# Performance work log

Hardware: AMD Instinct MI355X
Metric: run time of the kernel (lower is better)

The kernel has to match this reference:

```python
import jax, jax.numpy as jnp
import numpy as np

N = 100000      # nodes
E = 1600000     # edges (avg degree 16)
F_IN = 128      # node feature dim
F_OUT = 128     # GCN output dim


def setup_inputs() -> dict:
    key = jax.random.key(0)
    ks = jax.random.split(key, 11)
    s = 0.05  # weight scale to keep activations sane
    return {
        "x": jax.random.normal(ks[0], (N, F_IN), jnp.float32),
        "edge_index": jax.random.randint(ks[1], (2, E), 0, N, jnp.int32),
        "W": jax.random.normal(ks[2], (F_IN, F_OUT), jnp.float32) * s,
        "p": jax.random.normal(ks[3], (F_IN,), jnp.float32),
        "w_ih": jax.random.normal(ks[4], (3 * F_OUT, F_IN), jnp.float32) * s,
        "w_hh": jax.random.normal(ks[5], (3 * F_OUT, F_OUT), jnp.float32) * s,
        "b_ih": jax.random.normal(ks[6], (3 * F_OUT,), jnp.float32) * s,
        "b_hh": jax.random.normal(ks[7], (3 * F_OUT,), jnp.float32) * s,
        "conv_bias": jax.random.normal(ks[8], (F_OUT,), jnp.float32) * s,
        "lin_w": jax.random.normal(ks[9], (1, F_OUT), jnp.float32) * s,
        "lin_b": jax.random.normal(ks[10], (1,), jnp.float32) * s,
    }


def reference(x, edge_index, W, p, w_ih, w_hh, b_ih, b_hh, conv_bias, lin_w, lin_b):
    n_nodes = x.shape[0]
    k, H = W.shape  # k = F_IN rows, H = F_OUT hidden size

    # --- TopK summarize: pick k nodes, gate by tanh(score) -> X_tilde [k, F_IN]
    scores = x @ p / jnp.linalg.norm(p)
    top_vals, top_idx = jax.lax.top_k(scores, k)
    x_tilde = x[top_idx] * jnp.tanh(top_vals)[:, None]

    # --- one GRU step evolving W (hidden state = rows of W)
    gi = x_tilde @ w_ih.T + b_ih   # [k, 3H]
    gh = W @ w_hh.T + b_hh         # [k, 3H]
    r = jax.nn.sigmoid(gi[:, :H] + gh[:, :H])
    z = jax.nn.sigmoid(gi[:, H:2 * H] + gh[:, H:2 * H])
    n = jnp.tanh(gi[:, 2 * H:] + r * gh[:, 2 * H:])
    W_new = (1.0 - z) * n + z * W  # [F_IN, F_OUT]

    # --- GCN conv with fixed W: sym-normalized adjacency with self loops
    row, col = edge_index[0], edge_index[1]
    deg = jax.ops.segment_sum(jnp.ones_like(row, dtype=x.dtype), col,
                              num_segments=n_nodes) + 1.0  # +1 for self loop
    dinv = jax.lax.rsqrt(deg)
    xw = x @ W_new                                   # [N, F_OUT]
    coef = dinv[row] * dinv[col]                     # [E]
    agg = jax.ops.segment_sum(xw[row] * coef[:, None], col, num_segments=n_nodes)
    agg = agg + xw * (dinv * dinv)[:, None] + conv_bias  # self-loop term + bias

    # --- head: ReLU + Linear(F_OUT, 1)
    h = jax.nn.relu(agg)
    return h @ lin_w.T + lin_b  # [N, 1]
```

## Files before the change

### kernel.cpp

```cpp
#include <hip/hip_runtime.h>
#include <math.h>

#define N_NODES 100000
#define N_EDGES 1600000
#define F 128

#define BSH 8
#define NBUCK 391
#define BCAP 5120
#define PB_EDGES 2048
#define NB_PART 782
#define NB_SCORES 6250
#define NB_COLLECT 392

typedef unsigned int u32;
typedef unsigned short u16;
typedef __attribute__((ext_vector_type(8))) short short8;
typedef __attribute__((ext_vector_type(4))) float floatx4;
typedef __attribute__((ext_vector_type(2))) float f32x2;


__device__ __forceinline__ u32 key_of(float s) {
    u32 u = __float_as_uint(s);
    return (u & 0x80000000u) ? ~u : (u | 0x80000000u);
}

__device__ __forceinline__ float wave_reduce(float v) {
    #pragma unroll
    for (int off = 32; off > 0; off >>= 1) v += __shfl_down(v, off, 64);
    return v;
}

__device__ __forceinline__ u16 f2bf(float f) {
    u32 u = __float_as_uint(f);
    u += 0x7fffu + ((u >> 16) & 1u);
    return (u16)(u >> 16);
}

__device__ __forceinline__ float bflo(u32 b) { return __uint_as_float(b << 16); }
__device__ __forceinline__ float bfhi(u32 b) { return __uint_as_float(b & 0xffff0000u); }

__device__ __forceinline__ void pk_acc(f32x2& acc, u32 u) {
    f32x2 v; v.x = bflo(u); v.y = bfhi(u);
    asm("v_pk_add_f32 %0, %1, %0" : "+v"(acc) : "v"(v));
}
__device__ __forceinline__ void pk_add2(f32x2& a, f32x2 b) {
    asm("v_pk_add_f32 %0, %1, %0" : "+v"(a) : "v"(b));
}


__global__ __launch_bounds__(256) void k_part(const int* __restrict__ ei,
                                              u32* __restrict__ gcur,
                                              u32* __restrict__ pairs) {
    __shared__ u32 lh[NBUCK];
    __shared__ u32 lbase[NBUCK];
    int t = threadIdx.x;
    int e0 = blockIdx.x * PB_EDGES;
    int e1 = e0 + PB_EDGES; if (e1 > N_EDGES) e1 = N_EDGES;
    for (int i = t; i < NBUCK; i += 256) lh[i] = 0u;
    __syncthreads();
    for (int e = e0 + t; e < e1; e += 256)
        atomicAdd(&lh[((u32)ei[N_EDGES + e]) >> BSH], 1u);
    __syncthreads();
    for (int b = t; b < NBUCK; b += 256) {
        u32 c = lh[b];
        lbase[b] = c ? atomicAdd(&gcur[b], c) : 0u;
        lh[b] = 0u;
    }
    __syncthreads();
    for (int e = e0 + t; e < e1; e += 256) {
        u32 d = (u32)ei[N_EDGES + e];
        u32 b = d >> BSH;
        u32 pos = lbase[b] + atomicAdd(&lh[b], 1u);
        pairs[(size_t)b * BCAP + pos] = ((d & 255u) << 17) | (u32)ei[e];
    }
}


__global__ __launch_bounds__(256) void k_scores(const float* __restrict__ x,
                                                const float* __restrict__ p,
                                                float* __restrict__ scores,
                                                u32* __restrict__ hist16) {
    int wave = threadIdx.x >> 6;
    int lane = threadIdx.x & 63;
    int q = lane >> 4, sub = lane & 15;
    int node = blockIdx.x * 16 + wave * 4 + q;
    const float* xr = &x[(size_t)node * F + sub * 8];
    float4 v0 = *(const float4*)xr;
    float4 v1 = *(const float4*)(xr + 4);
    float4 p0 = *(const float4*)&p[sub * 8];
    float4 p1 = *(const float4*)&p[sub * 8 + 4];
    float d = v0.x * p0.x + v0.y * p0.y + v0.z * p0.z + v0.w * p0.w
            + v1.x * p1.x + v1.y * p1.y + v1.z * p1.z + v1.w * p1.w;
    #pragma unroll
    for (int off = 1; off < 16; off <<= 1) d += __shfl_xor(d, off, 64);
    if (sub == 0) {
        scores[node] = d;
        atomicAdd(&hist16[key_of(d) >> 16], 1u);
    }
}


__global__ __launch_bounds__(1024) void k_scan16(const u32* __restrict__ hist16,
                                                 u32* __restrict__ state) {
    __shared__ u32 a[1024];
    int t = threadIdx.x;
    const uint4* h4 = (const uint4*)hist16;
    u32 local = 0;
    #pragma unroll
    for (int i = 0; i < 16; i++) {
        uint4 v = h4[t * 16 + i];
        local += v.x + v.y + v.z + v.w;
    }
    a[t] = local;
    __syncthreads();
    for (int off = 1; off < 1024; off <<= 1) {
        u32 add = (t + off < 1024) ? a[t + off] : 0u;
        __syncthreads();
        a[t] += add;
        __syncthreads();
    }
    u32 S_above = (t == 1023) ? 0u : a[t + 1];
    if (S_above < 128u && a[t] >= 128u) {
        u32 cum = S_above;
        for (int v = t * 64 + 63; v >= t * 64; v--) {
            cum += hist16[v];
            if (cum >= 128u) { state[0] = (u32)v; break; }
        }
    }
}


__global__ __launch_bounds__(256) void k_mid(const float* __restrict__ scores,
                                             u32* __restrict__ state,
                                             u32* __restrict__ cand,
                                             const u32* __restrict__ pairs,
                                             const u32* __restrict__ gcur,
                                             u32* __restrict__ offs,
                                             float* __restrict__ dinv,
                                             u32* __restrict__ ebuf) {
    if (blockIdx.x < NB_COLLECT) {
        u32 T = state[0] << 16;
        int i = blockIdx.x * 256 + threadIdx.x;
        if (i < N_NODES) {
            if (key_of(scores[i]) >= T) {
                u32 pos = atomicAdd(&state[2], 1u);
                if (pos < 2048u) cand[pos] = (u32)i;
            }
        }
    } else {
        __shared__ u32 h[256];
        __shared__ u32 sc[256];
        __shared__ u32 ps[512];
        int b = blockIdx.x - NB_COLLECT, t = threadIdx.x;
        ps[t]       = (t < NBUCK)       ? gcur[t]       : 0u;
        ps[t + 256] = (t + 256 < NBUCK) ? gcur[t + 256] : 0u;
        __syncthreads();
        for (int off = 1; off < 512; off <<= 1) {
            int i0 = t, i1 = t + 256;
            u32 v0 = (i0 >= off) ? ps[i0 - off] : 0u;
            u32 v1 = (i1 >= off) ? ps[i1 - off] : 0u;
            __syncthreads();
            ps[i0] += v0; ps[i1] += v1;
            __syncthreads();
        }
        u32 base = ps[b] - gcur[b];
        u32 cnt  = gcur[b];
        const u32* seg = pairs + (size_t)b * BCAP;
        u32 lo = (u32)b << BSH;
        h[t] = 0u;
        __syncthreads();
        for (u32 i = t; i < cnt; i += 256)
            atomicAdd(&h[seg[i] >> 17], 1u);
        __syncthreads();
        sc[t] = h[t];
        __syncthreads();
        for (int off = 1; off < 256; off <<= 1) {
            u32 v = (t >= off) ? sc[t - off] : 0u;
            __syncthreads();
            sc[t] += v;
            __syncthreads();
        }
        int nn = N_NODES - (int)lo;
        if (t < nn) {
            u32 c = h[t];
            offs[lo + t] = base + (sc[t] - c);
            dinv[lo + t] = rsqrtf((float)c + 1.0f);
        }
        u32 excl = sc[t] - h[t];
        __syncthreads();
        sc[t] = excl;
        __syncthreads();
        for (u32 i = t; i < cnt; i += 256) {
            u32 pr = seg[i];
            u32 pos = base + atomicAdd(&sc[pr >> 17], 1u);
            ebuf[pos] = pr & 0x1ffffu;
        }
        if (b == 0 && t == 0) offs[N_NODES] = N_EDGES;
    }
}

__global__ void k_assemble16(const float* __restrict__ scores, const float* __restrict__ p,
                             const u32* __restrict__ state, const u32* __restrict__ cand,
                             u32* __restrict__ top_idx, float* __restrict__ gate) {
    __shared__ u32 ci[2048];
    __shared__ float csc[2048];
    __shared__ float s_inv;
    int t = threadIdx.x;
    if (t < 64) {
        float2 pv = *(const float2*)&p[t * 2];
        float d = pv.x * pv.x + pv.y * pv.y;
        d = wave_reduce(d);
        if (t == 0) s_inv = rsqrtf(d);
    }
    u32 nc = state[2]; if (nc > 2048u) nc = 2048u;
    for (u32 i = t; i < nc; i += 256) { u32 ix = cand[i]; ci[i] = ix; csc[i] = scores[ix]; }
    __syncthreads();
    for (u32 i = t; i < nc; i += 256) {
        u32 myk = key_of(csc[i]);
        u32 myi = ci[i];
        int rank = 0;
        for (u32 j = 0; j < nc; j++) {
            u32 ok = key_of(csc[j]);
            rank += (int)((ok > myk) || (ok == myk && ci[j] < myi));
        }
        if (rank < 128) {
            top_idx[rank] = myi;
            gate[rank] = tanhf(csc[i] * s_inv);
        }
    }
}


__global__ __launch_bounds__(256) void k_ggemm(const float* __restrict__ x,
                                               const float* __restrict__ W,
                                               const float* __restrict__ w_ih,
                                               const float* __restrict__ w_hh,
                                               const u32* __restrict__ top_idx,
                                               const float* __restrict__ gate,
                                               float* __restrict__ G) {
    __shared__ float As[32][128];
    __shared__ float Bs[64][131];
    int t = threadIdx.x;
    int k0 = blockIdx.x * 32;
    int by = blockIdx.y;
    int j0 = by * 64;
    bool is_gi = (by < 6);
    #pragma unroll
    for (int i = 0; i < 4; i++) {
        int l = t + i * 256;
        int row = l >> 5, c4 = l & 31;
        float4 v;
        if (is_gi) {
            u32 idx = top_idx[k0 + row];
            float gt = gate[k0 + row];
            v = *(const float4*)&x[(size_t)idx * F + c4 * 4];
            v.x *= gt; v.y *= gt; v.z *= gt; v.w *= gt;
        } else {
            v = *(const float4*)&W[(k0 + row) * F + c4 * 4];
        }
        *(float4*)&As[row][c4 * 4] = v;
    }
    const float* mat = is_gi ? w_ih : w_hh;
    int jbase = is_gi ? j0 : (j0 - 384);
    #pragma unroll
    for (int i = 0; i < 8; i++) {
        int l = t + i * 256;
        int row = l >> 5, c4 = l & 31;
        float4 v = *(const float4*)&mat[(jbase + row) * F + c4 * 4];
        Bs[row][c4 * 4 + 0] = v.x; Bs[row][c4 * 4 + 1] = v.y;
        Bs[row][c4 * 4 + 2] = v.z; Bs[row][c4 * 4 + 3] = v.w;
    }
    __syncthreads();
    int ty = t >> 5, tx = t & 31;
    float acc[4][2] = {};
    #pragma unroll 4
    for (int f = 0; f < 128; f++) {
        float b0 = Bs[tx * 2][f], b1 = Bs[tx * 2 + 1][f];
        #pragma unroll
        for (int i = 0; i < 4; i++) {
            float a = As[ty * 4 + i][f];
            acc[i][0] += a * b0;
            acc[i][1] += a * b1;
        }
    }
    #pragma unroll
    for (int i = 0; i < 4; i++) {
        int k = k0 + ty * 4 + i;
        G[(size_t)k * 768 + j0 + tx * 2 + 0] = acc[i][0];
        G[(size_t)k * 768 + j0 + tx * 2 + 1] = acc[i][1];
    }
}


__global__ void k_gate(const float* __restrict__ G, const float* __restrict__ W,
                       const float* __restrict__ b_ih, const float* __restrict__ b_hh,
                       float* __restrict__ Wnew, u16* __restrict__ Bfrag) {
    int idx = blockIdx.x * blockDim.x + threadIdx.x;
    int k = idx >> 7, h = idx & 127;
    const float* gk = &G[(size_t)k * 768];
    float gir = gk[h]       + b_ih[h];
    float giz = gk[128 + h] + b_ih[128 + h];
    float gin = gk[256 + h] + b_ih[256 + h];
    float ghr = gk[384 + h] + b_hh[h];
    float ghz = gk[512 + h] + b_hh[128 + h];
    float ghn = gk[640 + h] + b_hh[256 + h];
    float wv  = W[k * F + h];
    float rg = 1.0f / (1.0f + expf(-(gir + ghr)));
    float z  = 1.0f / (1.0f + expf(-(giz + ghz)));
    float n  = tanhf(gin + rg * ghn);
    float val = (1.0f - z) * n + z * wv;
    Wnew[k * F + h] = val;
    int nb = h >> 4, kc = k >> 5, q = (k >> 3) & 3, m = h & 15, jj = k & 7;
    Bfrag[(((nb * 4 + kc) * 64) + q * 16 + m) * 8 + jj] = f2bf(val);
}


__global__ __launch_bounds__(256) void k_gemm(const float* __restrict__ x,
                                              const u16* __restrict__ Bfrag,
                                              const float* __restrict__ dinv,
                                              u16* __restrict__ yw) {
    __shared__ __align__(16) u16 As[8448];
    int t = threadIdx.x;
    int r0 = blockIdx.x * 64;
    #pragma unroll
    for (int i = 0; i < 8; i++) {
        int l = t + i * 256;
        int row = l >> 5, c4 = l & 31;
        int f0 = c4 * 4;
        float4 v = {0.f, 0.f, 0.f, 0.f};
        if (r0 + row < N_NODES) v = *(const float4*)&x[(size_t)(r0 + row) * F + f0];
        int widx = (((row >> 4) * 4 + (f0 >> 5)) * 64 + ((f0 >> 3) & 3) * 16 + (row & 15)) * 8
                   + (f0 & 7);
        ushort4 s4;
        s4.x = f2bf(v.x); s4.y = f2bf(v.y); s4.z = f2bf(v.z); s4.w = f2bf(v.w);
        *(ushort4*)&As[widx] = s4;
    }
    __syncthreads();

    int wv = t >> 6, lane = t & 63;
    int q = lane >> 4, m = lane & 15;
    floatx4 acc[8] = {};
    #pragma unroll
    for (int kc = 0; kc < 4; kc++) {
        short8 a = *(const short8*)&As[((wv * 4 + kc) * 64 + lane) * 8];
        #pragma unroll
        for (int nb = 0; nb < 8; nb++) {
            short8 bfr = *(const short8*)&Bfrag[((nb * 4 + kc) * 64 + lane) * 8];
            acc[nb] = __builtin_amdgcn_mfma_f32_16x16x32_bf16(a, bfr, acc[nb], 0, 0, 0);
        }
    }
    __syncthreads();

    float d[4];
    #pragma unroll
    for (int reg = 0; reg < 4; reg++) {
        int gr = r0 + wv * 16 + q * 4 + reg;
        d[reg] = (gr < N_NODES) ? dinv[gr] : 0.f;
    }
    #pragma unroll
    for (int nb = 0; nb < 8; nb++) {
        #pragma unroll
        for (int reg = 0; reg < 4; reg++) {
            int row = wv * 16 + q * 4 + reg;
            As[row * 132 + nb * 16 + m] = f2bf(acc[nb][reg] * d[reg]);
        }
    }
    __syncthreads();
    {
        int row = t >> 2, segi = t & 3;
        int gr = r0 + row;
        if (gr < N_NODES) {
            const uint2* src = (const uint2*)&As[row * 132 + segi * 32];
            uint2* dst = (uint2*)&yw[(size_t)gr * F + segi * 32];
            #pragma unroll
            for (int i = 0; i < 8; i++) dst[i] = src[i];
        }
    }
}


#define EDGE_GROUP(J) {                                                      \
    u32 r = ebuf[(J) + q];                                                   \
    uint4 bb = *(const uint4*)&yw32[(size_t)r * 64 + sub * 4];               \
    pk_acc(a01, bb.x); pk_acc(a23, bb.y);                                    \
    pk_acc(a45, bb.z); pk_acc(a67, bb.w); }

#define BFLY(A) {                                                            \
    f32x2 tb;                                                                \
    tb.x = __shfl_xor(A.x, 16, 64); tb.y = __shfl_xor(A.y, 16, 64);          \
    pk_add2(A, tb);                                                          \
    tb.x = __shfl_xor(A.x, 32, 64); tb.y = __shfl_xor(A.y, 32, 64);          \
    pk_add2(A, tb); }

__global__ void k_gather(const u32* __restrict__ yw32, const u32* __restrict__ offs,
                         const u32* __restrict__ ebuf, const float* __restrict__ dinv,
                         const float* __restrict__ conv_bias, const float* __restrict__ lin_w,
                         const float* __restrict__ lin_b, float* __restrict__ out) {
    int c = blockIdx.x * 4 + (threadIdx.x >> 6);
    if (c >= N_NODES) return;
    int lane = threadIdx.x & 63;
    int q = lane >> 4, sub = lane & 15;
    u32 jbeg = offs[c], jend = offs[c + 1];
    f32x2 a01 = {0.f, 0.f}, a23 = {0.f, 0.f}, a45 = {0.f, 0.f}, a67 = {0.f, 0.f};
    u32 j = jbeg;
    for (; j + 16 <= jend; j += 16) {
        EDGE_GROUP(j) EDGE_GROUP(j + 4) EDGE_GROUP(j + 8) EDGE_GROUP(j + 12)
    }
    for (; j + 4 <= jend; j += 4) EDGE_GROUP(j)
    u32 rem = jend - j;
    if (rem) {
        u32 idx = ((u32)q < rem) ? (j + q) : j;
        u32 r = ebuf[idx];
        uint4 bb = *(const uint4*)&yw32[(size_t)r * 64 + sub * 4];
        if ((u32)q < rem) {
            pk_acc(a01, bb.x); pk_acc(a23, bb.y);
            pk_acc(a45, bb.z); pk_acc(a67, bb.w);
        }
    }
    BFLY(a01) BFLY(a23) BFLY(a45) BFLY(a67)
    float dc = dinv[c];
    uint4 sb = *(const uint4*)&yw32[(size_t)c * 64 + sub * 4];
    float4 cb0 = *(const float4*)&conv_bias[sub * 8];
    float4 cb1 = *(const float4*)&conv_bias[sub * 8 + 4];
    float4 lw0 = *(const float4*)&lin_w[sub * 8];
    float4 lw1 = *(const float4*)&lin_w[sub * 8 + 4];
    float h0 = fmaxf(dc * (a01.x + bflo(sb.x)) + cb0.x, 0.f);
    float h1 = fmaxf(dc * (a01.y + bfhi(sb.x)) + cb0.y, 0.f);
    float h2 = fmaxf(dc * (a23.x + bflo(sb.y)) + cb0.z, 0.f);
    float h3 = fmaxf(dc * (a23.y + bfhi(sb.y)) + cb0.w, 0.f);
    float h4 = fmaxf(dc * (a45.x + bflo(sb.z)) + cb1.x, 0.f);
    float h5 = fmaxf(dc * (a45.y + bfhi(sb.z)) + cb1.y, 0.f);
    float h6 = fmaxf(dc * (a67.x + bflo(sb.w)) + cb1.z, 0.f);
    float h7 = fmaxf(dc * (a67.y + bfhi(sb.w)) + cb1.w, 0.f);
    float part = (h0 * lw0.x + h1 * lw0.y + h2 * lw0.z + h3 * lw0.w)
               + (h4 * lw1.x + h5 * lw1.y + h6 * lw1.z + h7 * lw1.w);
    #pragma unroll
    for (int off = 8; off > 0; off >>= 1) part += __shfl_down(part, off, 64);
    if (lane == 0) out[c] = part + lin_b[0];
}


extern "C" void kernel_launch(void* const* d_in, const int* in_sizes, int n_in,
                              void* d_out, int out_size, void* d_ws, size_t ws_size,
                              hipStream_t stream) {
    const float* x         = (const float*)d_in[0];
    const int*   ei        = (const int*)  d_in[1];
    const float* W         = (const float*)d_in[2];
    const float* p         = (const float*)d_in[3];
    const float* w_ih      = (const float*)d_in[4];
    const float* w_hh      = (const float*)d_in[5];
    const float* b_ih      = (const float*)d_in[6];
    const float* b_hh      = (const float*)d_in[7];
    const float* conv_bias = (const float*)d_in[8];
    const float* lin_w     = (const float*)d_in[9];
    const float* lin_b     = (const float*)d_in[10];
    float* out = (float*)d_out;

    u32*   w  = (u32*)d_ws;
    float* wf = (float*)d_ws;

    const size_t SCORES_W = 0;
    const size_t DINV_W   = 100096;
    const size_t OFFS_W   = 200192;
    const size_t HIST16_W = 300288;
    const size_t STATE_W  = 365824;
    const size_t GCUR_W   = 365832;
    const size_t CAND_W   = 366224;
    const size_t TOPI_W   = 368272;
    const size_t GATE_W   = 368400;
    const size_t WNEW_W   = 368528;
    const size_t BFRAG_W  = 384912;
    const size_t PAIRS_W  = 389008;
    const size_t EBUF_W   = 2400000;
    const size_t YW_W     = 4000000;

    float* scores  = wf + SCORES_W;
    float* dinv    = wf + DINV_W;
    u32*   offs    = w  + OFFS_W;
    u32*   hist16  = w  + HIST16_W;
    u32*   state   = w  + STATE_W;
    u32*   gcur    = w  + GCUR_W;
    u32*   cand    = w  + CAND_W;
    u32*   top_idx = w  + TOPI_W;
    float* gate    = wf + GATE_W;
    float* Wnew    = wf + WNEW_W;
    u16*   Bfrag   = (u16*)(w + BFRAG_W);
    u32*   pairs   = w  + PAIRS_W;
    float* G       = wf + PAIRS_W;
    u32*   ebuf    = w  + EBUF_W;
    u16*   yw      = (u16*)(w + YW_W);
    u32*   yw32    = w + YW_W;

    hipMemsetAsync(hist16, 0, (65536 + 8 + NBUCK) * sizeof(u32), stream);

    k_part<<<NB_PART, 256, 0, stream>>>(ei, gcur, pairs);
    k_scores<<<NB_SCORES, 256, 0, stream>>>(x, p, scores, hist16);
    k_scan16<<<1, 1024, 0, stream>>>(hist16, state);
    k_mid<<<NB_COLLECT + NBUCK, 256, 0, stream>>>(scores, state, cand, pairs, gcur,
                                                  offs, dinv, ebuf);
    k_assemble16<<<1, 256, 0, stream>>>(scores, p, state, cand, top_idx, gate);

    k_ggemm<<<dim3(4, 12), 256, 0, stream>>>(x, W, w_ih, w_hh, top_idx, gate, G);
    k_gate<<<64, 256, 0, stream>>>(G, W, b_ih, b_hh, Wnew, Bfrag);

    k_gemm<<<1563, 256, 0, stream>>>(x, Bfrag, dinv, yw);

    k_gather<<<25000, 256, 0, stream>>>(yw32, offs, ebuf, dinv, conv_bias, lin_w,
                                        lin_b, out);
}
```

Before: 328.0 us.

## Fuse edge partition with score pass and move top-k selection into one block

Merges the edge-bucketing and score kernels into one launch, and drops the global 16-bit histogram and its atomics. Top-k threshold selection now runs in a single 1024-thread block using two-level 12-bit radix histograms in shared memory, then collects candidates. A second block of the same launch computes the bucket prefix that k_mid previously recomputed in every block. This cuts kernel launches, the large memset and global atomics, but it puts a serial single-block pass over all 100k scores on the critical path.

```diff
diff --git a/kernel.cpp b/kernel.cpp
--- a/kernel.cpp
+++ b/kernel.cpp
@@ -10,8 +10,7 @@
 #define BCAP 5120
 #define PB_EDGES 2048
 #define NB_PART 782
-#define NB_SCORES 6250
-#define NB_COLLECT 392
+#define NB_SCORES 1563
 
 typedef unsigned int u32;
 typedef unsigned short u16;
@@ -49,174 +48,158 @@
 }
 
 
-__global__ __launch_bounds__(256) void k_part(const int* __restrict__ ei,
-                                              u32* __restrict__ gcur,
-                                              u32* __restrict__ pairs) {
-    __shared__ u32 lh[NBUCK];
-    __shared__ u32 lbase[NBUCK];
+__global__ void k_front(const float* __restrict__ x, const float* __restrict__ p,
+                        const int* __restrict__ ei, float* __restrict__ scores,
+                        u32* __restrict__ gcur, u32* __restrict__ pairs) {
+    if (blockIdx.x < NB_PART) {
+        __shared__ u32 lh[NBUCK];
+        __shared__ u32 lbase[NBUCK];
+        int t = threadIdx.x;
+        int e0 = blockIdx.x * PB_EDGES;
+        int e1 = e0 + PB_EDGES; if (e1 > N_EDGES) e1 = N_EDGES;
+        for (int i = t; i < NBUCK; i += 256) lh[i] = 0u;
+        __syncthreads();
+        for (int e = e0 + t; e < e1; e += 256)
+            atomicAdd(&lh[((u32)ei[N_EDGES + e]) >> BSH], 1u);
+        __syncthreads();
+        for (int b = t; b < NBUCK; b += 256) {
+            u32 c = lh[b];
+            lbase[b] = c ? atomicAdd(&gcur[b], c) : 0u;
+            lh[b] = 0u;
+        }
+        __syncthreads();
+        for (int e = e0 + t; e < e1; e += 256) {
+            u32 d = (u32)ei[N_EDGES + e];
+            u32 b = d >> BSH;
+            u32 pos = lbase[b] + atomicAdd(&lh[b], 1u);
+            pairs[(size_t)b * BCAP + pos] = ((d & 255u) << 17) | (u32)ei[e];
+        }
+    } else {
+        int sb = blockIdx.x - NB_PART;
+        int wave = threadIdx.x >> 6;
+        int lane = threadIdx.x & 63;
+        int q = lane >> 4, sub = lane & 15;
+        int nb0 = sb * 64 + wave * 16 + q;
+        float4 p0 = *(const float4*)&p[sub * 8];
+        float4 p1 = *(const float4*)&p[sub * 8 + 4];
+        #pragma unroll
+        for (int r = 0; r < 4; r++) {
+            int node = nb0 + r * 4;
+            if (node >= N_NODES) continue;
+            const float* xr = &x[(size_t)node * F + sub * 8];
+            float4 v0 = *(const float4*)xr;
+            float4 v1 = *(const float4*)(xr + 4);
+            float d = v0.x * p0.x + v0.y * p0.y + v0.z * p0.z + v0.w * p0.w
+                    + v1.x * p1.x + v1.y * p1.y + v1.z * p1.z + v1.w * p1.w;
+            #pragma unroll
+            for (int off = 1; off < 16; off <<= 1) d += __shfl_xor(d, off, 64);
+            if (sub == 0) scores[node] = d;
+        }
+    }
+}
+
+
+__global__ __launch_bounds__(1024) void k_select(const float* __restrict__ scores,
+                                                 const float* __restrict__ p,
+                                                 u32* __restrict__ top_idx,
+                                                 float* __restrict__ gate,
+                                                 const u32* __restrict__ gcur,
+                                                 u32* __restrict__ bbase) {
     int t = threadIdx.x;
-    int e0 = blockIdx.x * PB_EDGES;
-    int e1 = e0 + PB_EDGES; if (e1 > N_EDGES) e1 = N_EDGES;
-    for (int i = t; i < NBUCK; i += 256) lh[i] = 0u;
-    __syncthreads();
-    for (int e = e0 + t; e < e1; e += 256)
-        atomicAdd(&lh[((u32)ei[N_EDGES + e]) >> BSH], 1u);
-    __syncthreads();
-    for (int b = t; b < NBUCK; b += 256) {
-        u32 c = lh[b];
-        lbase[b] = c ? atomicAdd(&gcur[b], c) : 0u;
-        lh[b] = 0u;
-    }
-    __syncthreads();
-    for (int e = e0 + t; e < e1; e += 256) {
-        u32 d = (u32)ei[N_EDGES + e];
-        u32 b = d >> BSH;
-        u32 pos = lbase[b] + atomicAdd(&lh[b], 1u);
-        pairs[(size_t)b * BCAP + pos] = ((d & 255u) << 17) | (u32)ei[e];
-    }
-}
-
-
-__global__ __launch_bounds__(256) void k_scores(const float* __restrict__ x,
-                                                const float* __restrict__ p,
-                                                float* __restrict__ scores,
-                                                u32* __restrict__ hist16) {
-    int wave = threadIdx.x >> 6;
-    int lane = threadIdx.x & 63;
-    int q = lane >> 4, sub = lane & 15;
-    int node = blockIdx.x * 16 + wave * 4 + q;
-    const float* xr = &x[(size_t)node * F + sub * 8];
-    float4 v0 = *(const float4*)xr;
-    float4 v1 = *(const float4*)(xr + 4);
-    float4 p0 = *(const float4*)&p[sub * 8];
-    float4 p1 = *(const float4*)&p[sub * 8 + 4];
-    float d = v0.x * p0.x + v0.y * p0.y + v0.z * p0.z + v0.w * p0.w
-            + v1.x * p1.x + v1.y * p1.y + v1.z * p1.z + v1.w * p1.w;
-    #pragma unroll
-    for (int off = 1; off < 16; off <<= 1) d += __shfl_xor(d, off, 64);
-    if (sub == 0) {
-        scores[node] = d;
-        atomicAdd(&hist16[key_of(d) >> 16], 1u);
-    }
-}
-
-
-__global__ __launch_bounds__(1024) void k_scan16(const u32* __restrict__ hist16,
-                                                 u32* __restrict__ state) {
-    __shared__ u32 a[1024];
-    int t = threadIdx.x;
-    const uint4* h4 = (const uint4*)hist16;
-    u32 local = 0;
-    #pragma unroll
-    for (int i = 0; i < 16; i++) {
-        uint4 v = h4[t * 16 + i];
-        local += v.x + v.y + v.z + v.w;
-    }
-    a[t] = local;
-    __syncthreads();
-    for (int off = 1; off < 1024; off <<= 1) {
-        u32 add = (t + off < 1024) ? a[t + off] : 0u;
-        __syncthreads();
-        a[t] += add;
-        __syncthreads();
-    }
-    u32 S_above = (t == 1023) ? 0u : a[t + 1];
-    if (S_above < 128u && a[t] >= 128u) {
-        u32 cum = S_above;
-        for (int v = t * 64 + 63; v >= t * 64; v--) {
-            cum += hist16[v];
-            if (cum >= 128u) { state[0] = (u32)v; break; }
-        }
-    }
-}
-
-
-__global__ __launch_bounds__(256) void k_mid(const float* __restrict__ scores,
-                                             u32* __restrict__ state,
-                                             u32* __restrict__ cand,
-                                             const u32* __restrict__ pairs,
-                                             const u32* __restrict__ gcur,
-                                             u32* __restrict__ offs,
-                                             float* __restrict__ dinv,
-                                             u32* __restrict__ ebuf) {
-    if (blockIdx.x < NB_COLLECT) {
-        u32 T = state[0] << 16;
-        int i = blockIdx.x * 256 + threadIdx.x;
-        if (i < N_NODES) {
-            if (key_of(scores[i]) >= T) {
-                u32 pos = atomicAdd(&state[2], 1u);
-                if (pos < 2048u) cand[pos] = (u32)i;
-            }
-        }
-    } else {
-        __shared__ u32 h[256];
-        __shared__ u32 sc[256];
-        __shared__ u32 ps[512];
-        int b = blockIdx.x - NB_COLLECT, t = threadIdx.x;
-        ps[t]       = (t < NBUCK)       ? gcur[t]       : 0u;
-        ps[t + 256] = (t + 256 < NBUCK) ? gcur[t + 256] : 0u;
-        __syncthreads();
-        for (int off = 1; off < 512; off <<= 1) {
-            int i0 = t, i1 = t + 256;
-            u32 v0 = (i0 >= off) ? ps[i0 - off] : 0u;
-            u32 v1 = (i1 >= off) ? ps[i1 - off] : 0u;
+    if (blockIdx.x == 1) {
+        __shared__ u32 a[1024];
+        u32 v = (t < NBUCK) ? gcur[t] : 0u;
+        a[t] = v;
+        __syncthreads();
+        for (int off = 1; off < 1024; off <<= 1) {
+            u32 add = (t >= off) ? a[t - off] : 0u;
             __syncthreads();
-            ps[i0] += v0; ps[i1] += v1;
+            a[t] += add;
             __syncthreads();
         }
-        u32 base = ps[b] - gcur[b];
-        u32 cnt  = gcur[b];
-        const u32* seg = pairs + (size_t)b * BCAP;
-        u32 lo = (u32)b << BSH;
-        h[t] = 0u;
-        __syncthreads();
-        for (u32 i = t; i < cnt; i += 256)
-            atomicAdd(&h[seg[i] >> 17], 1u);
-        __syncthreads();
-        sc[t] = h[t];
-        __syncthreads();
-        for (int off = 1; off < 256; off <<= 1) {
-            u32 v = (t >= off) ? sc[t - off] : 0u;
-            __syncthreads();
-            sc[t] += v;
-            __syncthreads();
-        }
-        int nn = N_NODES - (int)lo;
-        if (t < nn) {
-            u32 c = h[t];
-            offs[lo + t] = base + (sc[t] - c);
-            dinv[lo + t] = rsqrtf((float)c + 1.0f);
-        }
-        u32 excl = sc[t] - h[t];
-        __syncthreads();
-        sc[t] = excl;
-        __syncthreads();
-        for (u32 i = t; i < cnt; i += 256) {
-            u32 pr = seg[i];
-            u32 pos = base + atomicAdd(&sc[pr >> 17], 1u);
-            ebuf[pos] = pr & 0x1ffffu;
-        }
-        if (b == 0 && t == 0) offs[N_NODES] = N_EDGES;
-    }
-}
-
-__global__ void k_assemble16(const float* __restrict__ scores, const float* __restrict__ p,
-                             const u32* __restrict__ state, const u32* __restrict__ cand,
-                             u32* __restrict__ top_idx, float* __restrict__ gate) {
+        if (t < NBUCK) bbase[t] = a[t] - v;
+        return;
+    }
+    __shared__ u32 hist[4096];
+    __shared__ u32 s1[1024];
     __shared__ u32 ci[2048];
     __shared__ float csc[2048];
     __shared__ float s_inv;
-    int t = threadIdx.x;
+    __shared__ u32 sb1, sabove1, st24, scnt;
     if (t < 64) {
         float2 pv = *(const float2*)&p[t * 2];
         float d = pv.x * pv.x + pv.y * pv.y;
         d = wave_reduce(d);
         if (t == 0) s_inv = rsqrtf(d);
     }
-    u32 nc = state[2]; if (nc > 2048u) nc = 2048u;
-    for (u32 i = t; i < nc; i += 256) { u32 ix = cand[i]; ci[i] = ix; csc[i] = scores[ix]; }
-    __syncthreads();
-    for (u32 i = t; i < nc; i += 256) {
+    if (t == 0) scnt = 0u;
+    #pragma unroll
+    for (int i = 0; i < 4; i++) hist[t * 4 + i] = 0u;
+    __syncthreads();
+    for (int i = t; i < N_NODES; i += 1024)
+        atomicAdd(&hist[key_of(scores[i]) >> 20], 1u);
+    __syncthreads();
+    s1[t] = hist[4 * t] + hist[4 * t + 1] + hist[4 * t + 2] + hist[4 * t + 3];
+    __syncthreads();
+    for (int off = 1; off < 1024; off <<= 1) {
+        u32 add = (t + off < 1024) ? s1[t + off] : 0u;
+        __syncthreads();
+        s1[t] += add;
+        __syncthreads();
+    }
+    {
+        u32 above = (t == 1023) ? 0u : s1[t + 1];
+        if (above < 128u && s1[t] >= 128u) {
+            u32 run = above;
+            for (int bin = 4 * t + 3; bin >= 4 * t; bin--) {
+                if (run + hist[bin] >= 128u) { sb1 = (u32)bin; sabove1 = run; break; }
+                run += hist[bin];
+            }
+        }
+    }
+    __syncthreads();
+    u32 b1 = sb1, above1 = sabove1;
+    #pragma unroll
+    for (int i = 0; i < 4; i++) hist[t * 4 + i] = 0u;
+    __syncthreads();
+    for (int i = t; i < N_NODES; i += 1024) {
+        u32 k = key_of(scores[i]);
+        if ((k >> 20) == b1) atomicAdd(&hist[(k >> 8) & 0xfffu], 1u);
+    }
+    __syncthreads();
+    s1[t] = hist[4 * t] + hist[4 * t + 1] + hist[4 * t + 2] + hist[4 * t + 3];
+    __syncthreads();
+    for (int off = 1; off < 1024; off <<= 1) {
+        u32 add = (t + off < 1024) ? s1[t + off] : 0u;
+        __syncthreads();
+        s1[t] += add;
+        __syncthreads();
+    }
+    {
+        u32 above = above1 + ((t == 1023) ? 0u : s1[t + 1]);
+        if (above < 128u && above1 + s1[t] >= 128u) {
+            u32 run = above;
+            for (int bin = 4 * t + 3; bin >= 4 * t; bin--) {
+                if (run + hist[bin] >= 128u) {
+                    st24 = (b1 << 12) | (u32)bin;
+                    break;
+                }
+                run += hist[bin];
+            }
+        }
+    }
+    __syncthreads();
+    u32 t24 = st24;
+    for (int i = t; i < N_NODES; i += 1024) {
+        u32 k = key_of(scores[i]);
+        if ((k >> 8) >= t24) {
+            u32 pos = atomicAdd(&scnt, 1u);
+            if (pos < 2048u) { ci[pos] = (u32)i; csc[pos] = scores[i]; }
+        }
+    }
+    __syncthreads();
+    u32 nc = scnt; if (nc > 2048u) nc = 2048u;
+    for (u32 i = t; i < nc; i += 1024) {
         u32 myk = key_of(csc[i]);
         u32 myi = ci[i];
         int rank = 0;
@@ -229,6 +212,51 @@
             gate[rank] = tanhf(csc[i] * s_inv);
         }
     }
+}
+
+
+__global__ __launch_bounds__(256) void k_mid(const u32* __restrict__ pairs,
+                                             const u32* __restrict__ gcur,
+                                             const u32* __restrict__ bbase,
+                                             u32* __restrict__ offs,
+                                             float* __restrict__ dinv,
+                                             u32* __restrict__ ebuf) {
+    __shared__ u32 h[256];
+    __shared__ u32 sc[256];
+    int b = blockIdx.x, t = threadIdx.x;
+    u32 base = bbase[b];
+    u32 cnt  = gcur[b];
+    const u32* seg = pairs + (size_t)b * BCAP;
+    u32 lo = (u32)b << BSH;
+    h[t] = 0u;
+    __syncthreads();
+    for (u32 i = t; i < cnt; i += 256)
+        atomicAdd(&h[seg[i] >> 17], 1u);
+    __syncthreads();
+    sc[t] = h[t];
+    __syncthreads();
+    for (int off = 1; off < 256; off <<= 1) {
+        u32 v = (t >= off) ? sc[t - off] : 0u;
+        __syncthreads();
+        sc[t] += v;
+        __syncthreads();
+    }
+    int nn = N_NODES - (int)lo;
+    if (t < nn) {
+        u32 c = h[t];
+        offs[lo + t] = base + (sc[t] - c);
+        dinv[lo + t] = rsqrtf((float)c + 1.0f);
+    }
+    u32 excl = sc[t] - h[t];
+    __syncthreads();
+    sc[t] = excl;
+    __syncthreads();
+    for (u32 i = t; i < cnt; i += 256) {
+        u32 pr = seg[i];
+        u32 pos = base + atomicAdd(&sc[pr >> 17], 1u);
+        ebuf[pos] = pr & 0x1ffffu;
+    }
+    if (b == 0 && t == 0) offs[N_NODES] = N_EDGES;
 }
 
 
@@ -463,25 +491,21 @@
     const size_t SCORES_W = 0;
     const size_t DINV_W   = 100096;
     const size_t OFFS_W   = 200192;
-    const size_t HIST16_W = 300288;
-    const size_t STATE_W  = 365824;
-    const size_t GCUR_W   = 365832;
-    const size_t CAND_W   = 366224;
-    const size_t TOPI_W   = 368272;
-    const size_t GATE_W   = 368400;
-    const size_t WNEW_W   = 368528;
-    const size_t BFRAG_W  = 384912;
-    const size_t PAIRS_W  = 389008;
+    const size_t GCUR_W   = 300288;
+    const size_t BBASE_W  = 300684;
+    const size_t TOPI_W   = 301080;
+    const size_t GATE_W   = 301208;
+    const size_t WNEW_W   = 301336;
+    const size_t BFRAG_W  = 317720;
+    const size_t PAIRS_W  = 321816;
     const size_t EBUF_W   = 2400000;
     const size_t YW_W     = 4000000;
 
     float* scores  = wf + SCORES_W;
     float* dinv    = wf + DINV_W;
     u32*   offs    = w  + OFFS_W;
-    u32*   hist16  = w  + HIST16_W;
-    u32*   state   = w  + STATE_W;
     u32*   gcur    = w  + GCUR_W;
-    u32*   cand    = w  + CAND_W;
+    u32*   bbase   = w  + BBASE_W;
     u32*   top_idx = w  + TOPI_W;
     float* gate    = wf + GATE_W;
     float* Wnew    = wf + WNEW_W;
@@ -492,15 +516,11 @@
     u16*   yw      = (u16*)(w + YW_W);
     u32*   yw32    = w + YW_W;
 
-    hipMemsetAsync(hist16, 0, (65536 + 8 + NBUCK) * sizeof(u32), stream);
-
-    k_part<<<NB_PART, 256, 0, stream>>>(ei, gcur, pairs);
-    k_scores<<<NB_SCORES, 256, 0, stream>>>(x, p, scores, hist16);
-    k_scan16<<<1, 1024, 0, stream>>>(hist16, state);
-    k_mid<<<NB_COLLECT + NBUCK, 256, 0, stream>>>(scores, state, cand, pairs, gcur,
-                                                  offs, dinv, ebuf);
-    k_assemble16<<<1, 256, 0, stream>>>(scores, p, state, cand, top_idx, gate);
-
+    hipMemsetAsync(gcur, 0, NBUCK * sizeof(u32), stream);
+
+    k_front<<<NB_PART + NB_SCORES, 256, 0, stream>>>(x, p, ei, scores, gcur, pairs);
+    k_select<<<2, 1024, 0, stream>>>(scores, p, top_idx, gate, gcur, bbase);
+    k_mid<<<NBUCK, 256, 0, stream>>>(pairs, gcur, bbase, offs, dinv, ebuf);
     k_ggemm<<<dim3(4, 12), 256, 0, stream>>>(x, W, w_ih, w_hh, top_idx, gate, G);
     k_gate<<<64, 256, 0, stream>>>(G, W, b_ih, b_hh, Wnew, Bfrag);
 
```

Result: no change. 326.8 us (-0.3%).
